# Kernel tuning notes

Hardware: AMD Instinct MI355X
Metric: run time of the kernel (lower is better)

Reference implementation:

```python
import jax, jax.numpy as jnp
import numpy as np

T, B, D, H = 1024, 64, 256, 256


def setup_inputs() -> dict:
    key = jax.random.key(0)
    ks = jax.random.split(key, 9)
    s = 1.0 / np.sqrt(D + H)  # roughly torch Linear init scale
    return {
        "inputs": jax.random.normal(ks[0], (T, B, D), dtype=jnp.float32),
        "Wf": jax.random.normal(ks[1], (H, D + H), dtype=jnp.float32) * s,
        "bf": jax.random.normal(ks[2], (H,), dtype=jnp.float32) * s,
        "Wi": jax.random.normal(ks[3], (H, D + H), dtype=jnp.float32) * s,
        "bi": jax.random.normal(ks[4], (H,), dtype=jnp.float32) * s,
        "Wg": jax.random.normal(ks[5], (H, D + H), dtype=jnp.float32) * s,
        "bg": jax.random.normal(ks[6], (H,), dtype=jnp.float32) * s,
        "Wo": jax.random.normal(ks[7], (H, D + H), dtype=jnp.float32) * s,
        "bo": jax.random.normal(ks[8], (H,), dtype=jnp.float32) * s,
    }


def reference(inputs, Wf, bf, Wi, bi, Wg, bg, Wo, bo):
    # inputs: [T, B, D]; torch Linear: y = x @ W.T + b
    Bsz = inputs.shape[1]
    h0 = jnp.zeros((Bsz, H), dtype=inputs.dtype)
    c0 = jnp.zeros((Bsz, H), dtype=inputs.dtype)

    def step(carry, x):
        hx, cx = carry
        comb = jnp.concatenate([x, hx], axis=1)  # [B, D+H]
        f = jax.nn.sigmoid(comb @ Wf.T + bf)
        i = jax.nn.sigmoid(comb @ Wi.T + bi)
        g = jnp.tanh(comb @ Wg.T + bg)
        o = jax.nn.sigmoid(comb @ Wo.T + bo)
        cx = f * cx + i * g
        hx = o * jnp.tanh(cx)
        return (hx, cx), hx

    (hx, cx), stacked = jax.lax.scan(step, (h0, c0), inputs)
    return stacked, hx, cx
```

## Files before the change

### kernel.cpp

```cpp
#include <hip/hip_runtime.h>
#include <cstdint>
#include <cstddef>

#define T_SEQ 1024
#define BATCH 64
#define DIM   256
#define HID   256
#define NG    (4*HID)
#define HPADN (HID + 8)

typedef _Float16 h2v __attribute__((ext_vector_type(2)));
union U16 { uint4 u; h2v h[4]; };

__device__ __forceinline__ float sigm_f(float x) {
    return 1.0f / (1.0f + __expf(-x));
}
__device__ __forceinline__ float tanh_f(float x) {
    x = fminf(fmaxf(x, -15.0f), 15.0f);
    float e = __expf(2.0f * x);
    return (e - 1.0f) / (e + 1.0f);
}

#define QP_XOR1(x) __int_as_float(__builtin_amdgcn_mov_dpp(__float_as_int(x), 0xB1, 0xf, 0xf, true))

__device__ __forceinline__ int hpad(int r) { return r + ((r >> 7) << 3); }

__global__ void pack_kernel(const float* __restrict__ Wf, const float* __restrict__ bf,
                            const float* __restrict__ Wi, const float* __restrict__ bi,
                            const float* __restrict__ Wg, const float* __restrict__ bg,
                            const float* __restrict__ Wo, const float* __restrict__ bo,
                            float* __restrict__ wx4, _Float16* __restrict__ whB,
                            float* __restrict__ bias4,
                            float* __restrict__ hstate, float* __restrict__ cstate) {
    int k = blockIdx.x;
    int j = threadIdx.x;
    int r = j & 255, g = j >> 8;
    const float* W  = (g == 0) ? Wf : (g == 1) ? Wi : (g == 2) ? Wg : Wo;
    const float* bb = (g == 0) ? bf : (g == 1) ? bi : (g == 2) ? bg : bo;
    int jp = r * 4 + g;
    wx4[(size_t)k * 1024 + jp] = W[(size_t)r * 512 + k];
    {
        int c = k >> 3, e = k & 7;
        int R = jp >> 2, s = jp & 3;
        int p = (c >= 16) ? 1 : 0;
        int lc = c - 16 * p;
        int t = 2 * R + p;
        size_t idx = (lc < 4)
            ? ((size_t)(lc * 4 + s) * 512 + t)
            : (8192 + (size_t)((lc - 4) * 4 + s) * 512 + t);
        whB[idx * 8 + e] = (_Float16)W[(size_t)r * 512 + 256 + k];
    }
    if (k == 0) bias4[jp] = bb[r];
    if (k < 64 && g == 0) hstate[k * 256 + r] = 0.0f;
    if (k < 64 && g == 1) cstate[k * 256 + r] = 0.0f;
}

__global__ __launch_bounds__(256) void xproj_kernel(
        const float* __restrict__ X, const float* __restrict__ wx4,
        const float* __restrict__ bias4, float4* __restrict__ xp) {
    __shared__ __align__(16) float xl[256 * 20];
    int tid = threadIdx.x;
    int R0 = blockIdx.x * 16;
    #pragma unroll
    for (int i = 0; i < 16; ++i)
        xl[tid * 20 + i] = X[(size_t)(R0 + i) * DIM + tid];
    __syncthreads();

    float4 bv = ((const float4*)bias4)[tid];
    float acc[16][4];
    #pragma unroll
    for (int i = 0; i < 16; ++i) {
        acc[i][0] = bv.x; acc[i][1] = bv.y; acc[i][2] = bv.z; acc[i][3] = bv.w;
    }
    const float4* __restrict__ wp = (const float4*)wx4 + tid;
    #pragma unroll 2
    for (int k = 0; k < 256; ++k) {
        float4 w  = wp[k << 8];
        float4 xa = *(const float4*)&xl[k * 20 + 0];
        float4 xb = *(const float4*)&xl[k * 20 + 4];
        float4 xc = *(const float4*)&xl[k * 20 + 8];
        float4 xd = *(const float4*)&xl[k * 20 + 12];
        float xr[16] = {xa.x, xa.y, xa.z, xa.w, xb.x, xb.y, xb.z, xb.w,
                        xc.x, xc.y, xc.z, xc.w, xd.x, xd.y, xd.z, xd.w};
        #pragma unroll
        for (int i = 0; i < 16; ++i) {
            acc[i][0] = fmaf(xr[i], w.x, acc[i][0]);
            acc[i][1] = fmaf(xr[i], w.y, acc[i][1]);
            acc[i][2] = fmaf(xr[i], w.z, acc[i][2]);
            acc[i][3] = fmaf(xr[i], w.w, acc[i][3]);
        }
    }
    #pragma unroll
    for (int i = 0; i < 16; ++i) {
        float4 v;
        v.x = acc[i][0]; v.y = acc[i][1]; v.z = acc[i][2]; v.w = acc[i][3];
        xp[(size_t)(R0 + i) * 256 + tid] = v;
    }
}

__global__ __launch_bounds__(512, 2) void lstm_step_kernel(
        const float* __restrict__ xp, const _Float16* __restrict__ whB,
        float* __restrict__ hstate, float* __restrict__ cstate,
        float* __restrict__ out, int t0, int Tc) {
    __shared__ __align__(16) _Float16 wl[16 * 512 * 8];
    __shared__ __align__(16) _Float16 hl[2][HPADN];
    int t = threadIdx.x, b = blockIdx.x;

    {
        const uint4* src = (const uint4*)whB;
        uint4* dst = (uint4*)wl;
        #pragma unroll
        for (int i = 0; i < 16; ++i)
            dst[i * 512 + t] = src[i * 512 + t];
    }
    uint4 wrg[12][4];
    {
        const uint4* src = (const uint4*)whB + 8192;
        #pragma unroll
        for (int i = 0; i < 12; ++i)
            #pragma unroll
            for (int s = 0; s < 4; ++s)
                wrg[i][s] = src[(size_t)((i * 4 + s) * 512) + t];
    }
    int podd = t & 1;
    float creg = cstate[b * HID + (t >> 1)];
    if (t < HID) hl[0][hpad(t)] = (_Float16)hstate[b * HID + t];
    float sm = podd ? 2.0f : 1.0f;
    float aa = sm, bbc = podd ? -1.0f : 0.0f;
    int hbase = (podd << 7) + (podd << 3);
    __syncthreads();

    const float2* __restrict__ xpf2 = (const float2*)xp;
    float2 xa2 = xpf2[(size_t)b * 512 + t];
    int cur = 0;
    for (int tt = 0; tt < Tc; ++tt) {
        int tn = (tt + 1 < Tc) ? tt + 1 : tt;
        float2 xn2 = xpf2[((size_t)tn * BATCH + b) * 512 + t];

        float sA0 = 0.f, sB0 = 0.f, sA1 = 0.f, sB1 = 0.f;
        float sA2 = 0.f, sB2 = 0.f, sA3 = 0.f, sB3 = 0.f;
        const _Float16* hb = &hl[cur][hbase];
        #pragma unroll
        for (int lc = 0; lc < 4; ++lc) {
            U16 h; h.u = *(const uint4*)&hb[lc * 8];
            U16 w0, w1, w2, w3;
            w0.u = *(const uint4*)&wl[((size_t)((lc * 4 + 0) * 512 + t)) * 8];
            w1.u = *(const uint4*)&wl[((size_t)((lc * 4 + 1) * 512 + t)) * 8];
            w2.u = *(const uint4*)&wl[((size_t)((lc * 4 + 2) * 512 + t)) * 8];
            w3.u = *(const uint4*)&wl[((size_t)((lc * 4 + 3) * 512 + t)) * 8];
            sA0 = __builtin_amdgcn_fdot2(w0.h[0], h.h[0], sA0, false);
            sB0 = __builtin_amdgcn_fdot2(w0.h[1], h.h[1], sB0, false);
            sA0 = __builtin_amdgcn_fdot2(w0.h[2], h.h[2], sA0, false);
            sB0 = __builtin_amdgcn_fdot2(w0.h[3], h.h[3], sB0, false);
            sA1 = __builtin_amdgcn_fdot2(w1.h[0], h.h[0], sA1, false);
            sB1 = __builtin_amdgcn_fdot2(w1.h[1], h.h[1], sB1, false);
            sA1 = __builtin_amdgcn_fdot2(w1.h[2], h.h[2], sA1, false);
            sB1 = __builtin_amdgcn_fdot2(w1.h[3], h.h[3], sB1, false);
            sA2 = __builtin_amdgcn_fdot2(w2.h[0], h.h[0], sA2, false);
            sB2 = __builtin_amdgcn_fdot2(w2.h[1], h.h[1], sB2, false);
            sA2 = __builtin_amdgcn_fdot2(w2.h[2], h.h[2], sA2, false);
            sB2 = __builtin_amdgcn_fdot2(w2.h[3], h.h[3], sB2, false);
            sA3 = __builtin_amdgcn_fdot2(w3.h[0], h.h[0], sA3, false);
            sB3 = __builtin_amdgcn_fdot2(w3.h[1], h.h[1], sB3, false);
            sA3 = __builtin_amdgcn_fdot2(w3.h[2], h.h[2], sA3, false);
            sB3 = __builtin_amdgcn_fdot2(w3.h[3], h.h[3], sB3, false);
        }
        #pragma unroll
        for (int i = 0; i < 12; ++i) {
            U16 h; h.u = *(const uint4*)&hb[(4 + i) * 8];
            U16 w0, w1, w2, w3;
            w0.u = wrg[i][0]; w1.u = wrg[i][1]; w2.u = wrg[i][2]; w3.u = wrg[i][3];
            sA0 = __builtin_amdgcn_fdot2(w0.h[0], h.h[0], sA0, false);
            sB0 = __builtin_amdgcn_fdot2(w0.h[1], h.h[1], sB0, false);
            sA0 = __builtin_amdgcn_fdot2(w0.h[2], h.h[2], sA0, false);
            sB0 = __builtin_amdgcn_fdot2(w0.h[3], h.h[3], sB0, false);
            sA1 = __builtin_amdgcn_fdot2(w1.h[0], h.h[0], sA1, false);
            sB1 = __builtin_amdgcn_fdot2(w1.h[1], h.h[1], sB1, false);
            sA1 = __builtin_amdgcn_fdot2(w1.h[2], h.h[2], sA1, false);
            sB1 = __builtin_amdgcn_fdot2(w1.h[3], h.h[3], sB1, false);
            sA2 = __builtin_amdgcn_fdot2(w2.h[0], h.h[0], sA2, false);
            sB2 = __builtin_amdgcn_fdot2(w2.h[1], h.h[1], sB2, false);
            sA2 = __builtin_amdgcn_fdot2(w2.h[2], h.h[2], sA2, false);
            sB2 = __builtin_amdgcn_fdot2(w2.h[3], h.h[3], sB2, false);
            sA3 = __builtin_amdgcn_fdot2(w3.h[0], h.h[0], sA3, false);
            sB3 = __builtin_amdgcn_fdot2(w3.h[1], h.h[1], sB3, false);
            sA3 = __builtin_amdgcn_fdot2(w3.h[2], h.h[2], sA3, false);
            sB3 = __builtin_amdgcn_fdot2(w3.h[3], h.h[3], sB3, false);
        }
        float P0 = sA0 + sB0, P1 = sA1 + sB1, P2 = sA2 + sB2, P3 = sA3 + sB3;
        float S0 = P0 + QP_XOR1(P0);
        float S1 = P1 + QP_XOR1(P1);
        float S2 = P2 + QP_XOR1(P2);
        float S3 = P3 + QP_XOR1(P3);
        float a0 = xa2.x + (podd ? S2 : S0);
        float a1 = xa2.y + (podd ? S3 : S1);
        float vA = fmaf(aa, sigm_f(sm * a0), bbc);
        float vB = sigm_f(a1);
        float eA = QP_XOR1(vA);
        float eB = QP_XOR1(vB);
        float f  = podd ? eA : vA;
        float ii = podd ? eB : vB;
        float gg = podd ? vA : eA;
        float o  = podd ? vB : eB;
        float c  = fmaf(f, creg, ii * gg);
        creg = c;
        float h  = o * tanh_f(c);
        if (!podd) hl[cur ^ 1][hpad(t >> 1)] = (_Float16)h;
        __syncthreads();
        if (t < HID)
            out[((size_t)(t0 + tt) * BATCH + b) * HID + t] = (float)hl[cur ^ 1][hpad(t)];
        xa2 = xn2;
        cur ^= 1;
    }
    if (t < HID) hstate[b * HID + t] = (float)hl[cur][hpad(t)];
    if (!podd)   cstate[b * HID + (t >> 1)] = creg;
}

__global__ void tail_kernel(const float* __restrict__ hstate,
                            const float* __restrict__ cstate, float* __restrict__ out) {
    int b = blockIdx.x, r = threadIdx.x;
    size_t base = (size_t)T_SEQ * BATCH * HID;
    out[base + b * HID + r] = hstate[b * HID + r];
    out[base + (size_t)BATCH * HID + b * HID + r] = cstate[b * HID + r];
}

extern "C" void kernel_launch(void* const* d_in, const int* in_sizes, int n_in,
                              void* d_out, int out_size, void* d_ws, size_t ws_size,
                              hipStream_t stream) {
    (void)in_sizes; (void)n_in; (void)out_size;
    const float* X  = (const float*)d_in[0];
    const float* Wf = (const float*)d_in[1];
    const float* bf = (const float*)d_in[2];
    const float* Wi = (const float*)d_in[3];
    const float* bi = (const float*)d_in[4];
    const float* Wg = (const float*)d_in[5];
    const float* bg = (const float*)d_in[6];
    const float* Wo = (const float*)d_in[7];
    const float* bo = (const float*)d_in[8];
    float* out = (float*)d_out;
    char*  ws  = (char*)d_ws;

    const size_t MB = 1 << 20, KB = 1 << 10;
    float*    wx4    = (float*)(ws);
    _Float16* whB    = (_Float16*)(ws + MB);
    float*    bias4  = (float*)(ws + MB + 512 * KB);
    float*    hstate = (float*)(ws + MB + 576 * KB);
    float*    cstate = (float*)(ws + MB + 640 * KB);
    float4*   xproj  = (float4*)(ws + 2 * MB);

    size_t fixed = 2 * MB;
    int Tc = 1024;
    while (Tc > 16 && fixed + (size_t)Tc * BATCH * NG * 4 > ws_size) Tc >>= 1;

    pack_kernel<<<256, 1024, 0, stream>>>(Wf, bf, Wi, bi, Wg, bg, Wo, bo,
                                          wx4, whB, bias4, hstate, cstate);
    for (int t0 = 0; t0 < T_SEQ; t0 += Tc) {
        xproj_kernel<<<Tc * BATCH / 16, 256, 0, stream>>>(
            X + (size_t)t0 * BATCH * DIM, wx4, bias4, xproj);
        lstm_step_kernel<<<BATCH, 512, 0, stream>>>(
            (const float*)xproj, whB, hstate, cstate, out, t0, Tc);
    }
    tail_kernel<<<BATCH, HID, 0, stream>>>(hstate, cstate, out);
}
```

Baseline: 2.011 ms.

## Overlap next chunk's input projection with recurrent steps in fused kernel

Splits the sequence into chunks and double-buffers the input-projection workspace. Each launch runs the 64 recurrent blocks for the current chunk alongside extra blocks that compute the projection for the next chunk, with shared memory unioned between the two roles. The aim is to hide the projection GEMM behind the latency-bound recurrence on idle CUs, in exchange for more launches, a smaller chunk size and possible contention for memory bandwidth with the recurrent blocks.

After: 1.751 ms. 1.15x faster.

```diff
diff --git a/kernel.cpp b/kernel.cpp
--- a/kernel.cpp
+++ b/kernel.cpp
@@ -98,13 +98,65 @@
     }
 }
 
-__global__ __launch_bounds__(512, 2) void lstm_step_kernel(
-        const float* __restrict__ xp, const _Float16* __restrict__ whB,
+struct RecSh { _Float16 wl[16 * 512 * 8]; _Float16 hl[2][HPADN]; };
+struct XpSh  { float xl[2][256 * 20]; };
+union FusedSh { RecSh rec; XpSh xpj; };
+
+__global__ __launch_bounds__(512, 2) void lstm_fused_kernel(
+        const float* __restrict__ xp_read, float4* __restrict__ xp_write,
+        const float* __restrict__ Xnext, const float* __restrict__ wx4,
+        const float* __restrict__ bias4, const _Float16* __restrict__ whB,
         float* __restrict__ hstate, float* __restrict__ cstate,
         float* __restrict__ out, int t0, int Tc) {
-    __shared__ __align__(16) _Float16 wl[16 * 512 * 8];
-    __shared__ __align__(16) _Float16 hl[2][HPADN];
-    int t = threadIdx.x, b = blockIdx.x;
+    __shared__ __align__(16) FusedSh sh;
+    int t = threadIdx.x;
+
+    if (blockIdx.x >= BATCH) {
+        int vb = blockIdx.x - BATCH;
+        int half = t >> 8;
+        int tid = t & 255;
+        int R0 = vb * 32 + half * 16;
+        float* xl = sh.xpj.xl[half];
+        #pragma unroll
+        for (int i = 0; i < 16; ++i)
+            xl[tid * 20 + i] = Xnext[(size_t)(R0 + i) * DIM + tid];
+        __syncthreads();
+
+        float4 bv = ((const float4*)bias4)[tid];
+        float acc[16][4];
+        #pragma unroll
+        for (int i = 0; i < 16; ++i) {
+            acc[i][0] = bv.x; acc[i][1] = bv.y; acc[i][2] = bv.z; acc[i][3] = bv.w;
+        }
+        const float4* __restrict__ wp = (const float4*)wx4 + tid;
+        #pragma unroll 2
+        for (int k = 0; k < 256; ++k) {
+            float4 w  = wp[k << 8];
+            float4 xa = *(const float4*)&xl[k * 20 + 0];
+            float4 xb = *(const float4*)&xl[k * 20 + 4];
+            float4 xc = *(const float4*)&xl[k * 20 + 8];
+            float4 xd = *(const float4*)&xl[k * 20 + 12];
+            float xr[16] = {xa.x, xa.y, xa.z, xa.w, xb.x, xb.y, xb.z, xb.w,
+                            xc.x, xc.y, xc.z, xc.w, xd.x, xd.y, xd.z, xd.w};
+            #pragma unroll
+            for (int i = 0; i < 16; ++i) {
+                acc[i][0] = fmaf(xr[i], w.x, acc[i][0]);
+                acc[i][1] = fmaf(xr[i], w.y, acc[i][1]);
+                acc[i][2] = fmaf(xr[i], w.z, acc[i][2]);
+                acc[i][3] = fmaf(xr[i], w.w, acc[i][3]);
+            }
+        }
+        #pragma unroll
+        for (int i = 0; i < 16; ++i) {
+            float4 v;
+            v.x = acc[i][0]; v.y = acc[i][1]; v.z = acc[i][2]; v.w = acc[i][3];
+            xp_write[(size_t)(R0 + i) * 256 + tid] = v;
+        }
+        return;
+    }
+
+    _Float16* wl = sh.rec.wl;
+    int b = blockIdx.x;
 
     {
         const uint4* src = (const uint4*)whB;
@@ -124,13 +176,13 @@
     }
     int podd = t & 1;
     float creg = cstate[b * HID + (t >> 1)];
-    if (t < HID) hl[0][hpad(t)] = (_Float16)hstate[b * HID + t];
+    if (t < HID) sh.rec.hl[0][hpad(t)] = (_Float16)hstate[b * HID + t];
     float sm = podd ? 2.0f : 1.0f;
     float aa = sm, bbc = podd ? -1.0f : 0.0f;
     int hbase = (podd << 7) + (podd << 3);
     __syncthreads();
 
-    const float2* __restrict__ xpf2 = (const float2*)xp;
+    const float2* __restrict__ xpf2 = (const float2*)xp_read;
     float2 xa2 = xpf2[(size_t)b * 512 + t];
     int cur = 0;
     for (int tt = 0; tt < Tc; ++tt) {
@@ -139,7 +191,7 @@
 
         float sA0 = 0.f, sB0 = 0.f, sA1 = 0.f, sB1 = 0.f;
         float sA2 = 0.f, sB2 = 0.f, sA3 = 0.f, sB3 = 0.f;
-        const _Float16* hb = &hl[cur][hbase];
+        const _Float16* hb = &sh.rec.hl[cur][hbase];
         #pragma unroll
         for (int lc = 0; lc < 4; ++lc) {
             U16 h; h.u = *(const uint4*)&hb[lc * 8];
@@ -205,14 +257,14 @@
         float c  = fmaf(f, creg, ii * gg);
         creg = c;
         float h  = o * tanh_f(c);
-        if (!podd) hl[cur ^ 1][hpad(t >> 1)] = (_Float16)h;
+        if (!podd) sh.rec.hl[cur ^ 1][hpad(t >> 1)] = (_Float16)h;
         __syncthreads();
         if (t < HID)
-            out[((size_t)(t0 + tt) * BATCH + b) * HID + t] = (float)hl[cur ^ 1][hpad(t)];
+            out[((size_t)(t0 + tt) * BATCH + b) * HID + t] = (float)sh.rec.hl[cur ^ 1][hpad(t)];
         xa2 = xn2;
         cur ^= 1;
     }
-    if (t < HID) hstate[b * HID + t] = (float)hl[cur][hpad(t)];
+    if (t < HID) hstate[b * HID + t] = (float)sh.rec.hl[cur][hpad(t)];
     if (!podd)   cstate[b * HID + (t >> 1)] = creg;
 }
 
@@ -246,19 +298,24 @@
     float*    bias4  = (float*)(ws + MB + 512 * KB);
     float*    hstate = (float*)(ws + MB + 576 * KB);
     float*    cstate = (float*)(ws + MB + 640 * KB);
-    float4*   xproj  = (float4*)(ws + 2 * MB);
-
-    size_t fixed = 2 * MB;
-    int Tc = 1024;
-    while (Tc > 16 && fixed + (size_t)Tc * BATCH * NG * 4 > ws_size) Tc >>= 1;
+
+    int Tc = 256;
+    while (Tc > 16 && 2 * MB + 2 * (size_t)Tc * BATCH * NG * 4 > ws_size) Tc >>= 1;
+    int Nc = T_SEQ / Tc;
+    size_t xpBytes = (size_t)Tc * BATCH * NG * 4;
+    float4* xpA = (float4*)(ws + 2 * MB);
+    float4* xpB = (float4*)(ws + 2 * MB + xpBytes);
 
     pack_kernel<<<256, 1024, 0, stream>>>(Wf, bf, Wi, bi, Wg, bg, Wo, bo,
                                           wx4, whB, bias4, hstate, cstate);
-    for (int t0 = 0; t0 < T_SEQ; t0 += Tc) {
-        xproj_kernel<<<Tc * BATCH / 16, 256, 0, stream>>>(
-            X + (size_t)t0 * BATCH * DIM, wx4, bias4, xproj);
-        lstm_step_kernel<<<BATCH, 512, 0, stream>>>(
-            (const float*)xproj, whB, hstate, cstate, out, t0, Tc);
+    xproj_kernel<<<Tc * BATCH / 16, 256, 0, stream>>>(X, wx4, bias4, xpA);
+    for (int i = 0; i < Nc; ++i) {
+        float4* rd = (i & 1) ? xpB : xpA;
+        float4* wr = (i & 1) ? xpA : xpB;
+        int nxp = (i < Nc - 1) ? (Tc * BATCH / 32) : 0;
+        lstm_fused_kernel<<<BATCH + nxp, 512, 0, stream>>>(
+            (const float*)rd, wr, X + (size_t)(i + 1) * Tc * BATCH * DIM,
+            wx4, bias4, whB, hstate, cstate, out, i * Tc, Tc);
     }
     tail_kernel<<<BATCH, HID, 0, stream>>>(hstate, cstate, out);
 }
```
